# Kernel optimization log

Hardware: AMD Instinct MI355X
Metric: run time of the kernel (lower is better)

## Reference

```python
import jax, jax.numpy as jnp
import numpy as np

LOG_CLAMP = -100.0  # torch BCE clamps log terms at -100


def _weights_from_target(target):
    # target: [B, 1, W, W]; weight[b,i,j] = W / (sqrt((i-x)^2 + (j-y)^2) + 1)
    # where (x, y) is the mean location of the per-sample max of target.
    B = target.shape[0]
    W = target.shape[-1]
    t = target.reshape(B, W, W)
    m = jnp.max(t, axis=(1, 2), keepdims=True)
    mask = (t == m).astype(t.dtype)                      # all argmax locations
    cnt = jnp.sum(mask, axis=(1, 2))                     # [B]
    idx = jnp.arange(W, dtype=t.dtype)
    x = jnp.sum(mask * idx[None, :, None], axis=(1, 2)) / cnt  # mean row index
    y = jnp.sum(mask * idx[None, None, :], axis=(1, 2)) / cnt  # mean col index
    a = idx[None, :, None] - x[:, None, None]            # [B, W, 1]
    b = idx[None, None, :] - y[:, None, None]            # [B, 1, W]
    dist = (jnp.sqrt(a * a + b * b) + 1.0) / W           # [B, W, W]
    return (1.0 / dist).reshape(target.shape)


def reference(input, target):
    weights = _weights_from_target(target)
    log_p = jnp.maximum(jnp.log(input), LOG_CLAMP)
    log_1mp = jnp.maximum(jnp.log1p(-input), LOG_CLAMP)
    bce = -(target * log_p + (1.0 - target) * log_1mp)
    return jnp.mean(weights * bce)


def setup_inputs() -> dict:
    key = jax.random.key(0)
    k1, k2 = jax.random.split(key)
    shape = (256, 1, 224, 224)
    # BCE requires probabilities in (0,1); keep strictly inside via small margin.
    input = jax.random.uniform(k1, shape, dtype=jnp.float32, minval=1e-4, maxval=1.0 - 1e-4)
    target = jax.random.uniform(k2, shape, dtype=jnp.float32)
    return {"input": input, "target": target}
```

## Files before the change

kernel.cpp:

```cpp
#include <hip/hip_runtime.h>
#include <math.h>


#define WIMG 224
#define WW (WIMG * WIMG)
#define NQ (WW / 4)
#define NB 256
#define NTHREADS 1024
#define LOG_CLAMP -100.0f
#define LN2 0.69314718055994530942f

__device__ __forceinline__ float fast_log(float x) {
    return __builtin_amdgcn_logf(x) * LN2;
}

__global__ __launch_bounds__(NTHREADS) void floss_kernel(
    const float* __restrict__ input,
    const float* __restrict__ target,
    float* __restrict__ out,
    float inv_total)
{
    const int b   = blockIdx.x;
    const int tid = threadIdx.x;
    const float4* __restrict__ t4 = (const float4*)(target + (size_t)b * WW);
    const float4* __restrict__ p4 = (const float4*)(input  + (size_t)b * WW);

    float m = -1.0f, cnt = 0.0f, si = 0.0f, sj = 0.0f;
    for (int q = tid; q < NQ; q += NTHREADS) {
        float4 v = t4[q];
        int i  = q / 56;
        int j0 = (q - i * 56) * 4;
        float fi = (float)i;
        float vv[4] = {v.x, v.y, v.z, v.w};
        #pragma unroll
        for (int k = 0; k < 4; ++k) {
            float val = vv[k];
            float fj  = (float)(j0 + k);
            if (val > m)       { m = val; cnt = 1.0f; si = fi; sj = fj; }
            else if (val == m) { cnt += 1.0f; si += fi; sj += fj; }
        }
    }
    #pragma unroll
    for (int off = 32; off > 0; off >>= 1) {
        float m2  = __shfl_down(m,   off);
        float c2  = __shfl_down(cnt, off);
        float si2 = __shfl_down(si,  off);
        float sj2 = __shfl_down(sj,  off);
        if (m2 > m)       { m = m2; cnt = c2; si = si2; sj = sj2; }
        else if (m2 == m) { cnt += c2; si += si2; sj += sj2; }
    }
    __shared__ float sm[16], sc[16], ssi[16], ssj[16];
    __shared__ float sxy[2];
    const int lane = tid & 63, wid = tid >> 6;
    if (lane == 0) { sm[wid] = m; sc[wid] = cnt; ssi[wid] = si; ssj[wid] = sj; }
    __syncthreads();
    if (tid == 0) {
        float M = sm[0], C = sc[0], SI = ssi[0], SJ = ssj[0];
        #pragma unroll
        for (int w = 1; w < 16; ++w) {
            float mw = sm[w];
            if (mw > M)       { M = mw; C = sc[w]; SI = ssi[w]; SJ = ssj[w]; }
            else if (mw == M) { C += sc[w]; SI += ssi[w]; SJ += ssj[w]; }
        }
        sxy[0] = SI / C;
        sxy[1] = SJ / C;
    }
    __syncthreads();
    const float x = sxy[0], y = sxy[1];

    float acc = 0.0f;
    for (int q = tid; q < NQ; q += NTHREADS) {
        float4 tv = t4[q];
        float4 pv = p4[q];
        int i  = q / 56;
        int j0 = (q - i * 56) * 4;
        float di  = (float)i - x;
        float di2 = di * di;
        float tt[4] = {tv.x, tv.y, tv.z, tv.w};
        float pp[4] = {pv.x, pv.y, pv.z, pv.w};
        #pragma unroll
        for (int k = 0; k < 4; ++k) {
            float dj = (float)(j0 + k) - y;
            float s   = __builtin_amdgcn_sqrtf(di2 + dj * dj);
            float wgt = (float)WIMG * __builtin_amdgcn_rcpf(s + 1.0f);
            float p = pp[k], t = tt[k];
            float lp  = fmaxf(fast_log(p),        LOG_CLAMP);
            float l1p = fmaxf(fast_log(1.0f - p), LOG_CLAMP);
            float bce = -(t * lp + (1.0f - t) * l1p);
            acc += wgt * bce;
        }
    }
    #pragma unroll
    for (int off = 32; off > 0; off >>= 1) acc += __shfl_down(acc, off);
    __shared__ float sred[16];
    if (lane == 0) sred[wid] = acc;
    __syncthreads();
    if (tid == 0) {
        float s = 0.0f;
        #pragma unroll
        for (int w = 0; w < 16; ++w) s += sred[w];
        atomicAdd(out, s * inv_total);
    }
}

extern "C" void kernel_launch(void* const* d_in, const int* in_sizes, int n_in,
                              void* d_out, int out_size, void* d_ws, size_t ws_size,
                              hipStream_t stream) {
    const float* input  = (const float*)d_in[0];
    const float* target = (const float*)d_in[1];
    float* out = (float*)d_out;
    hipMemsetAsync(out, 0, sizeof(float), stream);
    const float inv_total = 1.0f / (256.0f * 224.0f * 224.0f);
    floss_kernel<<<NB, NTHREADS, 0, stream>>>(input, target, out, inv_total);
}
```

Baseline: 124.0 us.

## Split into centroid, BCE, and final-reduce kernels with more blocks

Splits the fused kernel into three launches. The first computes each sample's argmax centroid into workspace. The second runs the BCE over 1024 blocks (four per sample) writing partial sums, and the third reduces those partials deterministically in place of the atomicAdd and memset. It also makes the argmax update branchless and folds the ln2 and negation constants into the weight, working in log2 space. The intent is better occupancy than 256 blocks on a GPU with many CUs, at the cost of extra launches and a second read of target.

```diff
diff --git a/kernel.cpp b/kernel.cpp
--- a/kernel.cpp
+++ b/kernel.cpp
@@ -6,27 +6,23 @@
 #define WW (WIMG * WIMG)
 #define NQ (WW / 4)
 #define NB 256
-#define NTHREADS 1024
-#define LOG_CLAMP -100.0f
+#define K1_THREADS 1024
+#define NPARTB 4
+#define QPB (NQ / NPARTB)
+#define K2_THREADS 512
+#define NPART (NB * NPARTB)
 #define LN2 0.69314718055994530942f
+#define CLAMP2 (-144.269504088896340736f)
 
-__device__ __forceinline__ float fast_log(float x) {
-    return __builtin_amdgcn_logf(x) * LN2;
-}
-
-__global__ __launch_bounds__(NTHREADS) void floss_kernel(
-    const float* __restrict__ input,
-    const float* __restrict__ target,
-    float* __restrict__ out,
-    float inv_total)
+__global__ __launch_bounds__(K1_THREADS) void centroid_kernel(
+    const float* __restrict__ target, float* __restrict__ xy)
 {
     const int b   = blockIdx.x;
     const int tid = threadIdx.x;
     const float4* __restrict__ t4 = (const float4*)(target + (size_t)b * WW);
-    const float4* __restrict__ p4 = (const float4*)(input  + (size_t)b * WW);
 
     float m = -1.0f, cnt = 0.0f, si = 0.0f, sj = 0.0f;
-    for (int q = tid; q < NQ; q += NTHREADS) {
+    for (int q = tid; q < NQ; q += K1_THREADS) {
         float4 v = t4[q];
         int i  = q / 56;
         int j0 = (q - i * 56) * 4;
@@ -36,8 +32,12 @@
         for (int k = 0; k < 4; ++k) {
             float val = vv[k];
             float fj  = (float)(j0 + k);
-            if (val > m)       { m = val; cnt = 1.0f; si = fi; sj = fj; }
-            else if (val == m) { cnt += 1.0f; si += fi; sj += fj; }
+            bool gt = val > m;
+            bool eq = val == m;
+            cnt = gt ? 1.0f : (cnt + (eq ? 1.0f : 0.0f));
+            si  = gt ? fi   : (si  + (eq ? fi   : 0.0f));
+            sj  = gt ? fj   : (sj  + (eq ? fj   : 0.0f));
+            m   = fmaxf(m, val);
         }
     }
     #pragma unroll
@@ -46,11 +46,13 @@
         float c2  = __shfl_down(cnt, off);
         float si2 = __shfl_down(si,  off);
         float sj2 = __shfl_down(sj,  off);
-        if (m2 > m)       { m = m2; cnt = c2; si = si2; sj = sj2; }
-        else if (m2 == m) { cnt += c2; si += si2; sj += sj2; }
+        bool gt = m2 > m, eq = m2 == m;
+        cnt = gt ? c2  : (cnt + (eq ? c2  : 0.0f));
+        si  = gt ? si2 : (si  + (eq ? si2 : 0.0f));
+        sj  = gt ? sj2 : (sj  + (eq ? sj2 : 0.0f));
+        m   = fmaxf(m, m2);
     }
     __shared__ float sm[16], sc[16], ssi[16], ssj[16];
-    __shared__ float sxy[2];
     const int lane = tid & 63, wid = tid >> 6;
     if (lane == 0) { sm[wid] = m; sc[wid] = cnt; ssi[wid] = si; ssj[wid] = sj; }
     __syncthreads();
@@ -59,17 +61,37 @@
         #pragma unroll
         for (int w = 1; w < 16; ++w) {
             float mw = sm[w];
-            if (mw > M)       { M = mw; C = sc[w]; SI = ssi[w]; SJ = ssj[w]; }
-            else if (mw == M) { C += sc[w]; SI += ssi[w]; SJ += ssj[w]; }
+            bool gt = mw > M, eq = mw == M;
+            C  = gt ? sc[w]  : (C  + (eq ? sc[w]  : 0.0f));
+            SI = gt ? ssi[w] : (SI + (eq ? ssi[w] : 0.0f));
+            SJ = gt ? ssj[w] : (SJ + (eq ? ssj[w] : 0.0f));
+            M  = fmaxf(M, mw);
         }
-        sxy[0] = SI / C;
-        sxy[1] = SJ / C;
+        xy[2 * b]     = SI / C;
+        xy[2 * b + 1] = SJ / C;
     }
-    __syncthreads();
-    const float x = sxy[0], y = sxy[1];
+}
+
+__global__ __launch_bounds__(K2_THREADS) void bce_kernel(
+    const float* __restrict__ input,
+    const float* __restrict__ target,
+    const float* __restrict__ xy,
+    float* __restrict__ partial)
+{
+    const int blk  = blockIdx.x;
+    const int b    = blk >> 2;
+    const int part = blk & 3;
+    const int tid  = threadIdx.x;
+    const float x = xy[2 * b];
+    const float y = xy[2 * b + 1];
+    const float4* __restrict__ t4 = (const float4*)(target + (size_t)b * WW);
+    const float4* __restrict__ p4 = (const float4*)(input  + (size_t)b * WW);
+    const int qbase = part * QPB;
+    const float Kc = -(float)WIMG * LN2;
 
     float acc = 0.0f;
-    for (int q = tid; q < NQ; q += NTHREADS) {
+    for (int ql = tid; ql < QPB; ql += K2_THREADS) {
+        int q  = qbase + ql;
         float4 tv = t4[q];
         float4 pv = p4[q];
         int i  = q / 56;
@@ -81,25 +103,44 @@
         #pragma unroll
         for (int k = 0; k < 4; ++k) {
             float dj = (float)(j0 + k) - y;
-            float s   = __builtin_amdgcn_sqrtf(di2 + dj * dj);
-            float wgt = (float)WIMG * __builtin_amdgcn_rcpf(s + 1.0f);
+            float s  = __builtin_amdgcn_sqrtf(di2 + dj * dj);
+            float wf = Kc * __builtin_amdgcn_rcpf(s + 1.0f);
             float p = pp[k], t = tt[k];
-            float lp  = fmaxf(fast_log(p),        LOG_CLAMP);
-            float l1p = fmaxf(fast_log(1.0f - p), LOG_CLAMP);
-            float bce = -(t * lp + (1.0f - t) * l1p);
-            acc += wgt * bce;
+            float lp2  = fmaxf(__builtin_amdgcn_logf(p),        CLAMP2);
+            float l1p2 = fmaxf(__builtin_amdgcn_logf(1.0f - p), CLAMP2);
+            acc += wf * (l1p2 + t * (lp2 - l1p2));
         }
     }
     #pragma unroll
     for (int off = 32; off > 0; off >>= 1) acc += __shfl_down(acc, off);
+    __shared__ float sred[8];
+    const int lane = tid & 63, wid = tid >> 6;
+    if (lane == 0) sred[wid] = acc;
+    __syncthreads();
+    if (tid == 0) {
+        float ssum = 0.0f;
+        #pragma unroll
+        for (int w = 0; w < 8; ++w) ssum += sred[w];
+        partial[blk] = ssum;
+    }
+}
+
+__global__ __launch_bounds__(NPART) void final_reduce(
+    const float* __restrict__ partial, float* __restrict__ out, float inv_total)
+{
+    const int tid = threadIdx.x;
+    float v = partial[tid];
+    #pragma unroll
+    for (int off = 32; off > 0; off >>= 1) v += __shfl_down(v, off);
     __shared__ float sred[16];
-    if (lane == 0) sred[wid] = acc;
+    const int lane = tid & 63, wid = tid >> 6;
+    if (lane == 0) sred[wid] = v;
     __syncthreads();
     if (tid == 0) {
         float s = 0.0f;
         #pragma unroll
         for (int w = 0; w < 16; ++w) s += sred[w];
-        atomicAdd(out, s * inv_total);
+        out[0] = s * inv_total;
     }
 }
 
@@ -109,7 +150,11 @@
     const float* input  = (const float*)d_in[0];
     const float* target = (const float*)d_in[1];
     float* out = (float*)d_out;
-    hipMemsetAsync(out, 0, sizeof(float), stream);
+    float* xy      = (float*)d_ws;
+    float* partial = (float*)d_ws + 512;
+
+    centroid_kernel<<<NB, K1_THREADS, 0, stream>>>(target, xy);
+    bce_kernel<<<NPART, K2_THREADS, 0, stream>>>(input, target, xy, partial);
     const float inv_total = 1.0f / (256.0f * 224.0f * 224.0f);
-    floss_kernel<<<NB, NTHREADS, 0, stream>>>(input, target, out, inv_total);
+    final_reduce<<<1, NPART, 0, stream>>>(partial, out, inv_total);
 }
```

Measured after the change: 125.3 us. Within noise of the previous version (+1.0%).

## Cache target in registers as fp16 to avoid re-reading it in the loss pass

Applied to the files above, without the earlier changes.

The first pass now keeps each thread's target values in registers, packed as half2, so the second pass no longer reads target from global memory a second time. The max/argmax update becomes branchless selects, the loops are fully unrolled with an explicit tail, and the log base-2 conversion and negation are folded into one weight constant. The intent is to cut global traffic, which the second target read roughly increases by half. The costs are extra register pressure and fp16 rounding of target in the BCE sum, which could alter accuracy slightly.

```diff
diff --git a/kernel.cpp b/kernel.cpp
--- a/kernel.cpp
+++ b/kernel.cpp
@@ -1,4 +1,5 @@
 #include <hip/hip_runtime.h>
+#include <hip/hip_fp16.h>
 #include <math.h>
 
 
@@ -6,15 +7,24 @@
 #define WW (WIMG * WIMG)
 #define NQ (WW / 4)
 #define NB 256
-#define NTHREADS 1024
-#define LOG_CLAMP -100.0f
+#define NT 1024
+#define NIT (NQ / NT)
+#define REM (NQ - NIT * NT)
 #define LN2 0.69314718055994530942f
+#define CLAMP2 (-144.269504088896340736f)
 
-__device__ __forceinline__ float fast_log(float x) {
-    return __builtin_amdgcn_logf(x) * LN2;
+__device__ __forceinline__ void stat_upd(float val, float fi, float fj,
+                                         float& m, float& cnt, float& si, float& sj)
+{
+    bool gt = val > m;
+    bool eq = val == m;
+    cnt = gt ? 1.0f : (cnt + (eq ? 1.0f : 0.0f));
+    si  = gt ? fi   : (si  + (eq ? fi   : 0.0f));
+    sj  = gt ? fj   : (sj  + (eq ? fj   : 0.0f));
+    m   = fmaxf(m, val);
 }
 
-__global__ __launch_bounds__(NTHREADS) void floss_kernel(
+__global__ __launch_bounds__(NT, 4) void floss_kernel(
     const float* __restrict__ input,
     const float* __restrict__ target,
     float* __restrict__ out,
@@ -26,28 +36,47 @@
     const float4* __restrict__ p4 = (const float4*)(input  + (size_t)b * WW);
 
     float m = -1.0f, cnt = 0.0f, si = 0.0f, sj = 0.0f;
-    for (int q = tid; q < NQ; q += NTHREADS) {
+    __half2 tc[2 * (NIT + 1)];
+    #pragma unroll
+    for (int it = 0; it < NIT; ++it) {
+        int q = it * NT + tid;
         float4 v = t4[q];
         int i  = q / 56;
         int j0 = (q - i * 56) * 4;
         float fi = (float)i;
-        float vv[4] = {v.x, v.y, v.z, v.w};
-        #pragma unroll
-        for (int k = 0; k < 4; ++k) {
-            float val = vv[k];
-            float fj  = (float)(j0 + k);
-            if (val > m)       { m = val; cnt = 1.0f; si = fi; sj = fj; }
-            else if (val == m) { cnt += 1.0f; si += fi; sj += fj; }
-        }
+        stat_upd(v.x, fi, (float)(j0 + 0), m, cnt, si, sj);
+        stat_upd(v.y, fi, (float)(j0 + 1), m, cnt, si, sj);
+        stat_upd(v.z, fi, (float)(j0 + 2), m, cnt, si, sj);
+        stat_upd(v.w, fi, (float)(j0 + 3), m, cnt, si, sj);
+        tc[2 * it]     = __floats2half2_rn(v.x, v.y);
+        tc[2 * it + 1] = __floats2half2_rn(v.z, v.w);
     }
+    const bool has_tail = tid < REM;
+    const int qt = NIT * NT + tid;
+    if (has_tail) {
+        float4 v = t4[qt];
+        int i  = qt / 56;
+        int j0 = (qt - i * 56) * 4;
+        float fi = (float)i;
+        stat_upd(v.x, fi, (float)(j0 + 0), m, cnt, si, sj);
+        stat_upd(v.y, fi, (float)(j0 + 1), m, cnt, si, sj);
+        stat_upd(v.z, fi, (float)(j0 + 2), m, cnt, si, sj);
+        stat_upd(v.w, fi, (float)(j0 + 3), m, cnt, si, sj);
+        tc[2 * NIT]     = __floats2half2_rn(v.x, v.y);
+        tc[2 * NIT + 1] = __floats2half2_rn(v.z, v.w);
+    }
+
     #pragma unroll
     for (int off = 32; off > 0; off >>= 1) {
         float m2  = __shfl_down(m,   off);
         float c2  = __shfl_down(cnt, off);
         float si2 = __shfl_down(si,  off);
         float sj2 = __shfl_down(sj,  off);
-        if (m2 > m)       { m = m2; cnt = c2; si = si2; sj = sj2; }
-        else if (m2 == m) { cnt += c2; si += si2; sj += sj2; }
+        bool gt = m2 > m, eq = m2 == m;
+        cnt = gt ? c2  : (cnt + (eq ? c2  : 0.0f));
+        si  = gt ? si2 : (si  + (eq ? si2 : 0.0f));
+        sj  = gt ? sj2 : (sj  + (eq ? sj2 : 0.0f));
+        m   = fmaxf(m, m2);
     }
     __shared__ float sm[16], sc[16], ssi[16], ssj[16];
     __shared__ float sxy[2];
@@ -59,47 +88,55 @@
         #pragma unroll
         for (int w = 1; w < 16; ++w) {
             float mw = sm[w];
-            if (mw > M)       { M = mw; C = sc[w]; SI = ssi[w]; SJ = ssj[w]; }
-            else if (mw == M) { C += sc[w]; SI += ssi[w]; SJ += ssj[w]; }
+            bool gt = mw > M, eq = mw == M;
+            C  = gt ? sc[w]  : (C  + (eq ? sc[w]  : 0.0f));
+            SI = gt ? ssi[w] : (SI + (eq ? ssi[w] : 0.0f));
+            SJ = gt ? ssj[w] : (SJ + (eq ? ssj[w] : 0.0f));
+            M  = fmaxf(M, mw);
         }
         sxy[0] = SI / C;
         sxy[1] = SJ / C;
     }
     __syncthreads();
     const float x = sxy[0], y = sxy[1];
+    const float Kc = -(float)WIMG * LN2;
 
     float acc = 0.0f;
-    for (int q = tid; q < NQ; q += NTHREADS) {
-        float4 tv = t4[q];
+    #pragma unroll
+    for (int it = 0; it <= NIT; ++it) {
+        int q = (it < NIT) ? (it * NT + tid) : qt;
+        if (it == NIT && !has_tail) break;
         float4 pv = p4[q];
+        float2 t01 = __half22float2(tc[2 * it]);
+        float2 t23 = __half22float2(tc[2 * it + 1]);
         int i  = q / 56;
         int j0 = (q - i * 56) * 4;
         float di  = (float)i - x;
         float di2 = di * di;
-        float tt[4] = {tv.x, tv.y, tv.z, tv.w};
+        float tt[4] = {t01.x, t01.y, t23.x, t23.y};
         float pp[4] = {pv.x, pv.y, pv.z, pv.w};
         #pragma unroll
         for (int k = 0; k < 4; ++k) {
             float dj = (float)(j0 + k) - y;
-            float s   = __builtin_amdgcn_sqrtf(di2 + dj * dj);
-            float wgt = (float)WIMG * __builtin_amdgcn_rcpf(s + 1.0f);
+            float s  = __builtin_amdgcn_sqrtf(di2 + dj * dj);
+            float wf = Kc * __builtin_amdgcn_rcpf(s + 1.0f);
             float p = pp[k], t = tt[k];
-            float lp  = fmaxf(fast_log(p),        LOG_CLAMP);
-            float l1p = fmaxf(fast_log(1.0f - p), LOG_CLAMP);
-            float bce = -(t * lp + (1.0f - t) * l1p);
-            acc += wgt * bce;
+            float lp2  = fmaxf(__builtin_amdgcn_logf(p),        CLAMP2);
+            float l1p2 = fmaxf(__builtin_amdgcn_logf(1.0f - p), CLAMP2);
+            acc += wf * (l1p2 + t * (lp2 - l1p2));
         }
     }
+
     #pragma unroll
     for (int off = 32; off > 0; off >>= 1) acc += __shfl_down(acc, off);
     __shared__ float sred[16];
     if (lane == 0) sred[wid] = acc;
     __syncthreads();
     if (tid == 0) {
-        float s = 0.0f;
+        float ssum = 0.0f;
         #pragma unroll
-        for (int w = 0; w < 16; ++w) s += sred[w];
-        atomicAdd(out, s * inv_total);
+        for (int w = 0; w < 16; ++w) ssum += sred[w];
+        atomicAdd(out, ssum * inv_total);
     }
 }
 
@@ -111,5 +148,5 @@
     float* out = (float*)d_out;
     hipMemsetAsync(out, 0, sizeof(float), stream);
     const float inv_total = 1.0f / (256.0f * 224.0f * 224.0f);
-    floss_kernel<<<NB, NTHREADS, 0, stream>>>(input, target, out, inv_total);
+    floss_kernel<<<NB, NT, 0, stream>>>(input, target, out, inv_total);
 }
```

After: 137.5 us. 10.9% more time.
